# Kernel optimization log

Hardware: AMD Instinct MI355X
Metric: run time of the kernel (lower is better)

The kernel has to match this reference:

```python
import jax, jax.numpy as jnp
import numpy as np

T, A, E, RAW, H, NACT, NTP = 64, 48, 22, 512, 256, 21, 3
# entity_distinct: self entity [0], friendly entities [1:12], hostile entities [12:22]
PARAM_SHAPES = [
    ("W1", (NTP, RAW, H)), ("b1", (NTP, H)), ("W2", (NTP, H, H)), ("b2", (NTP, H)),
    ("WCf", (NTP, 2 * H, H)), ("bCf", (NTP, H)), ("WMf", (NTP, 2 * H + 2 * RAW, H)), ("bMf", (NTP, H)),
    ("WCh", (NTP, 2 * H, H)), ("bCh", (NTP, H)), ("WMh", (NTP, 2 * H + 2 * RAW, H)), ("bMh", (NTP, H)),
    ("L1", (NTP, 2 * H, H)), ("bL1", (NTP, H)), ("L2", (NTP, H, H // 2)), ("bL2", (NTP, H // 2)),
    ("L3", (NTP, H // 2, NACT)), ("bL3", (NTP, NACT)),
    ("V1", (NTP, 2 * H, H)), ("bV1", (NTP, H)), ("V2", (NTP, H, 1)), ("bV2", (NTP, 1)),
]
PNAMES = [n for n, _ in PARAM_SHAPES]


def setup_inputs() -> dict:
    key = jax.random.key(0)
    ks = jax.random.split(key, 3 + len(PARAM_SHAPES))
    inp = {
        "obs": jax.random.normal(ks[0], (T, A, E, RAW), jnp.float32),
        "hete_pick": jax.random.randint(ks[1], (T, A), 0, NTP, jnp.int32),
        "dead": jax.random.bernoulli(ks[2], 0.15, (T, A, E)),
    }
    for i, (n, s) in enumerate(PARAM_SHAPES):
        inp[n] = jax.random.normal(ks[3 + i], s, jnp.float32) * 0.02
    return inp


def _net_forward(p, obs, dead):
    relu = jax.nn.relu
    obs = jnp.where(dead[..., None], 0.0, obs)                    # nan_to_num for dead entities
    v = relu(obs @ p["W1"] + p["b1"]) @ p["W2"] + p["b2"]         # [T,A,E,H] per-entity encoder
    zs, ze_f, ze_h = obs[..., 0, :], obs[..., 1:12, :], obs[..., 12:22, :]
    vs, ve_f, ve_h = v[..., 0, :], v[..., 1:12, :], v[..., 12:22, :]
    df, dh = dead[..., 1:12], dead[..., 12:22]

    def conc(ve, d, ze, WC, bC, WM, bM):
        w = (~d).astype(obs.dtype)                                # alive mask [T,A,Ef]
        denom = jnp.maximum(w.sum(-1, keepdims=True), 1.0)
        pool = jnp.einsum('taeh,tae->tah', ve, w) / denom         # masked mean over entities
        pool_z = jnp.einsum('taer,tae->tar', ze, w) / denom       # skip-connect raw-obs pool
        vC = relu(jnp.concatenate([vs, pool], -1) @ WC + bC)
        vM = relu(jnp.concatenate([vs, pool, zs, pool_z], -1) @ WM + bM)
        return vC, vM

    vfC, vfM = conc(ve_f, df, ze_f, p["WCf"], p["bCf"], p["WMf"], p["bMf"])
    vhC, vhM = conc(ve_h, dh, ze_h, p["WCh"], p["bCh"], p["WMh"], p["bMh"])
    vC = jnp.concatenate([vfC, vhC], -1)                          # [T,A,2H] dual-conc fuse
    vM = jnp.concatenate([vfM, vhM], -1)
    logits = relu(relu(vC @ p["L1"] + p["bL1"]) @ p["L2"] + p["bL2"]) @ p["L3"] + p["bL3"]
    value = relu(vM @ p["V1"] + p["bV1"]) @ p["V2"] + p["bV2"]    # [T,A,1]
    logp = jax.nn.log_softmax(logits, -1)
    act = jnp.argmax(logits, -1)                                  # deterministic (test_mode) action
    alp = jnp.take_along_axis(logp, act[..., None], -1)           # [T,A,1] action log-prob
    return act, value, alp


def reference(obs, hete_pick, dead, W1, b1, W2, b2, WCf, bCf, WMf, bMf, WCh, bCh, WMh, bMh,
              L1, bL1, L2, bL2, L3, bL3, V1, bV1, V2, bV2):
    params = dict(W1=W1, b1=b1, W2=W2, b2=b2, WCf=WCf, bCf=bCf, WMf=WMf, bMf=bMf,
                  WCh=WCh, bCh=bCh, WMh=WMh, bMh=bMh, L1=L1, bL1=bL1, L2=L2, bL2=bL2,
                  L3=L3, bL3=bL3, V1=V1, bV1=bV1, V2=V2, bV2=bV2)
    act = jnp.zeros((T, A), jnp.int32)
    value = jnp.zeros((T, A, 1), obs.dtype)
    alp = jnp.zeros((T, A, 1), obs.dtype)
    for t in range(NTP):                                          # heterogeneous dispatch (distribute_compute)
        pt = {k: v[t] for k, v in params.items()}
        a_t, v_t, lp_t = _net_forward(pt, obs, dead)
        m = hete_pick == t                                        # mask_arr[t]
        act = jnp.where(m, a_t.astype(jnp.int32), act)
        value = jnp.where(m[..., None], v_t, value)
        alp = jnp.where(m[..., None], lp_t, alp)
    return act, value, alp
```

## Files before the change

### kernel.cpp

```cpp
#include <hip/hip_runtime.h>
#include <cstdint>

#define T_ 64
#define A_ 48
#define NP_ 3072
#define E_ 22
#define RAW_ 512
#define H_ 256
#define NACT_ 21
#define NTP_ 3
#define PV_ 3456
#define RV_ 68096
#define NDEAD_ 67584

typedef unsigned short u16;
typedef __attribute__((ext_vector_type(8))) short short8;
typedef __attribute__((ext_vector_type(4))) short short4v;
typedef __attribute__((ext_vector_type(4))) float floatx4;

__device__ __forceinline__ u16 f2bf(float x) {
    unsigned r;
    asm("v_cvt_pk_bf16_f32 %0, %1, %1" : "=v"(r) : "v"(x));
    return (u16)r;
}
__device__ __forceinline__ float bf2f(u16 h) {
    return __uint_as_float(((unsigned)h) << 16);
}

typedef __attribute__((address_space(1))) const void* gp_t;
typedef __attribute__((address_space(3))) void* lp_t;
__device__ __forceinline__ void gload16(const void* g, void* l) {
    __builtin_amdgcn_global_load_lds((gp_t)g, (lp_t)l, 16, 0, 0);
}

__device__ __forceinline__ floatx4 ld_f4(const float* p) {
    floatx4 r;
    asm volatile("global_load_dwordx4 %0, %1, off" : "=&v"(r) : "v"(p));
    return r;
}
__device__ __forceinline__ short8 ld_s8(const u16* p) {
    short8 r;
    asm volatile("global_load_dwordx4 %0, %1, off" : "=&v"(r) : "v"(p));
    return r;
}
template<int N>
__device__ __forceinline__ void wait_vm_f(floatx4 (&a)[4]) {
    asm volatile("s_waitcnt vmcnt(%4)"
                 : "+v"(a[0]), "+v"(a[1]), "+v"(a[2]), "+v"(a[3])
                 : "i"(N) : "memory");
}
template<int N>
__device__ __forceinline__ void wait_vm_s(short8 (&a)[4]) {
    asm volatile("s_waitcnt vmcnt(%4)"
                 : "+v"(a[0]), "+v"(a[1]), "+v"(a[2]), "+v"(a[3])
                 : "i"(N) : "memory");
}

__device__ __forceinline__ int swzk(int r) { return ((r >> 1) ^ r) & 3; }

__global__ void k_bucket(const unsigned* __restrict__ deadRaw,
                         const int* __restrict__ hete, int* __restrict__ wsI)
{
    __shared__ int fl[2];
    __shared__ int sc[3], cur[3], sps[3], srs[3];
    int tid = threadIdx.x;
    if (tid < 2) fl[tid] = 0;
    if (tid < 3) { sc[tid] = 0; cur[tid] = 0; }
    __syncthreads();
    int ni = 0, nf = 0;
    for (int i = tid; i < 1024; i += 256) {
        unsigned w = deadRaw[i];
        if (w > 1u) ni = 1;
        if (w != 0u && w != 0x3F800000u) nf = 1;
    }
    if (ni) atomicOr(&fl[0], 1);
    if (nf) atomicOr(&fl[1], 1);
    for (int p = tid; p < NP_; p += 256) atomicAdd(&sc[hete[p]], 1);
    __syncthreads();
    if (tid == 0) {
        int c0 = sc[0], c1 = sc[1], c2 = sc[2];
        int p1 = (c0 + 127) & ~127;
        int p2 = p1 + ((c1 + 127) & ~127);
        sps[0] = 0; sps[1] = p1; sps[2] = p2;
        int r1 = (22 * c0 + 127) & ~127;
        int r2 = r1 + ((22 * c1 + 127) & ~127);
        srs[0] = 0; srs[1] = r1; srs[2] = r2;
        wsI[0] = fl[0] ? (fl[1] ? 2 : 1) : 0;
        wsI[1] = c0; wsI[2] = c1; wsI[3] = c2;
        wsI[4] = 0; wsI[5] = p1; wsI[6] = p2;
        wsI[8] = 0; wsI[9] = r1; wsI[10] = r2;
    }
    __syncthreads();
    int* pairIdx = wsI + 16;
    int* prb = pairIdx + PV_;
    for (int pv = tid; pv < PV_; pv += 256) pairIdx[pv] = -1;
    __syncthreads();
    for (int p = tid; p < NP_; p += 256) {
        int t = hete[p];
        int pos = atomicAdd(&cur[t], 1);
        pairIdx[sps[t] + pos] = p;
    }
    for (int pv = tid; pv < PV_; pv += 256) {
        int t = (pv >= sps[1]) + (pv >= sps[2]);
        prb[pv] = srs[t] + 22 * (pv - sps[t]);
    }
}

__global__ void k_deadmask(const void* __restrict__ dead,
                           const int* __restrict__ wsI, float* __restrict__ dm)
{
    int i = blockIdx.x * 256 + threadIdx.x;
    if (i >= NDEAD_) return;
    int mode = wsI[0];
    bool d;
    if (mode == 0)      d = ((const int*)dead)[i] != 0;
    else if (mode == 1) d = ((const float*)dead)[i] != 0.f;
    else                d = ((const unsigned char*)dead)[i] != 0;
    dm[i] = d ? 0.f : 1.f;
}

__global__ void k_rowobs(const int* __restrict__ cnt, const int* __restrict__ ps,
                         const int* __restrict__ rs, const int* __restrict__ pairIdx,
                         const float* __restrict__ dm, int* __restrict__ rowObs)
{
    int rv = blockIdx.x * 256 + threadIdx.x;
    if (rv >= RV_) return;
    int t = (rv >= rs[1]) + (rv >= rs[2]);
    int local = rv - rs[t];
    int out = -1;
    if (local < 22 * cnt[t]) {
        int pl = local / 22;
        int e = local - pl * 22;
        int p = pairIdx[ps[t] + pl];
        if (p >= 0) {
            int oi = p * 22 + e;
            if (dm[oi] != 0.f) out = oi;
        }
    }
    rowObs[rv] = out;
}

struct WCA {
    const float* W[8]; u16* Hi[8]; u16* Lo[8]; int K[8]; int bs[9];
};
__global__ __launch_bounds__(256) void k_wconv(WCA a)
{
    int blk = blockIdx.x;
    int s = 0;
#pragma unroll
    for (int i = 1; i < 8; ++i) if (blk >= a.bs[i]) s = i;
    int lb = blk - a.bs[s];
    int K = a.K[s];
    int K8 = K >> 3;
    int kc = lb % K8;
    int t  = lb / K8;
    int n  = threadIdx.x;
    const float* w = a.W[s] + (long)t * K * 256 + n;
    short8 hv, lv;
#pragma unroll
    for (int j = 0; j < 8; ++j) {
        float x = w[(long)(kc * 8 + j) * 256];
        u16 hh = f2bf(x);
        hv[j] = (short)hh;
        lv[j] = (short)f2bf(x - bf2f(hh));
    }
    long o = ((long)t * 256 + n) * K + kc * 8;
    *(short8*)(a.Hi[s] + o) = hv;
    *(short8*)(a.Lo[s] + o) = lv;
}

struct GD {
    const void* Aa; const void* Ab;
    const u16* Bh; const u16* Bl;
    const float* bias;
    void* Ca; void* Cb;
    long lda; long ldc;
    int K; int coff;
};
struct GA4 { GD d[4]; };

template<int AMODE, bool RELU, int OUTS>
__global__ __launch_bounds__(256, 2) void k_mgemm(
    GA4 ga, const int* __restrict__ rowIdx, const int* __restrict__ starts)
{
    __shared__ short smem[32768];
    const int tid = threadIdx.x;
    const GD d = ga.d[blockIdx.z];
    const long rb = (long)blockIdx.x * 128;
    const int n0 = blockIdx.y * 128;
    const int t = (rb >= starts[0]) + (rb >= starts[1]);
    const int K = d.K;
    const long lda = d.lda;
    const u16* bhT = d.Bh + ((long)t * 256 + n0) * K;
    const u16* blT = d.Bl + ((long)t * 256 + n0) * K;
    const float* biasT = d.bias + (long)t * 256 + n0;

    const int cs = tid & 3;
    const int r0 = tid >> 2;
    const int r1 = 64 + r0;

    const int ar = tid >> 3;
    const int ac = (tid & 7) * 4;
    long arow[4]; float amask[4];
    const float* Afp = (const float*)d.Aa;
    if (AMODE == 1) {
#pragma unroll
        for (int it = 0; it < 4; ++it) {
            int r = 32 * it + ar;
            int i0 = rowIdx[rb + r];
            amask[it] = (i0 < 0) ? 0.f : 1.f;
            arow[it] = (i0 < 0) ? 0 : (long)i0 * lda;
        }
    }
    const u16* ahT = (const u16*)d.Aa;
    const u16* alT = (const u16*)d.Ab;

    const int wave = tid >> 6;
    const int lane = tid & 63;
    const int wr = (wave >> 1) * 64;
    const int wc = (wave & 1) * 64;
    const int lm = lane & 15;
    const int quad = lane >> 4;

    auto issueB = [&](int b, int k0) {
        short* Bh = smem + b * 16384 + 8192;
        short* Bl = smem + b * 16384 + 12288;
#pragma unroll
        for (int i = 0; i < 2; ++i) {
            int c = i * 256 + tid;
            int r = c >> 2;
            long go = (long)r * K + k0 + ((cs ^ swzk(r)) << 3);
            gload16(bhT + go, &Bh[c << 3]);
            gload16(blT + go, &Bl[c << 3]);
        }
    };
    auto issueA1 = [&](int k0, floatx4 (&dst)[4]) {
#pragma unroll
        for (int it = 0; it < 4; ++it)
            dst[it] = ld_f4(Afp + arow[it] + k0 + ac);
    };
    auto issueA0 = [&](int k0, short8 (&dst)[4]) {
        dst[0] = ld_s8(ahT + (rb + r0) * lda + k0 + cs * 8);
        dst[1] = ld_s8(ahT + (rb + r1) * lda + k0 + cs * 8);
        dst[2] = ld_s8(alT + (rb + r0) * lda + k0 + cs * 8);
        dst[3] = ld_s8(alT + (rb + r1) * lda + k0 + cs * 8);
    };
    auto writeA1 = [&](int b, floatx4 (&src)[4]) {
        short* AhW = smem + b * 16384;
        short* AlW = AhW + 4096;
#pragma unroll
        for (int it = 0; it < 4; ++it) {
            short4v hv, lv;
#pragma unroll
            for (int e = 0; e < 4; ++e) {
                float x = src[it][e] * amask[it];
                u16 hh = f2bf(x);
                hv[e] = (short)hh;
                lv[e] = (short)f2bf(x - bf2f(hh));
            }
            int r = 32 * it + ar;
            int bs = (((ac >> 3) ^ swzk(r)) << 4) | ((ac & 4) << 1);
            *(short4v*)((char*)AhW + r * 64 + bs) = hv;
            *(short4v*)((char*)AlW + r * 64 + bs) = lv;
        }
    };
    auto writeA0 = [&](int b, short8 (&src)[4]) {
        short* AhW = smem + b * 16384;
        short* AlW = AhW + 4096;
        *(short8*)((char*)AhW + r0 * 64 + ((cs ^ swzk(r0)) << 4)) = src[0];
        *(short8*)((char*)AhW + r1 * 64 + ((cs ^ swzk(r1)) << 4)) = src[1];
        *(short8*)((char*)AlW + r0 * 64 + ((cs ^ swzk(r0)) << 4)) = src[2];
        *(short8*)((char*)AlW + r1 * 64 + ((cs ^ swzk(r1)) << 4)) = src[3];
    };

    floatx4 acc[4][4];
#pragma unroll
    for (int i = 0; i < 4; ++i)
#pragma unroll
        for (int j = 0; j < 4; ++j) acc[i][j] = (floatx4){0.f, 0.f, 0.f, 0.f};

    auto computeT = [&](int b) {
        const short* Ah = smem + b * 16384;
        const short* Al = Ah + 4096;
        const short* Bh = Ah + 8192;
        const short* Bl = Ah + 12288;
        short8 fah[4], fal[4];
#pragma unroll
        for (int i = 0; i < 4; ++i) {
            int m = wr + 16 * i + lm;
            int sl = (quad ^ swzk(m)) << 3;
            fah[i] = *(const short8*)&Ah[(m << 5) + sl];
            fal[i] = *(const short8*)&Al[(m << 5) + sl];
        }
        __builtin_amdgcn_s_setprio(1);
#pragma unroll
        for (int j = 0; j < 4; ++j) {
            int n = wc + 16 * j + lm;
            int sl = (quad ^ swzk(n)) << 3;
            short8 fbh = *(const short8*)&Bh[(n << 5) + sl];
            short8 fbl = *(const short8*)&Bl[(n << 5) + sl];
#pragma unroll
            for (int i = 0; i < 4; ++i) {
                acc[i][j] = __builtin_amdgcn_mfma_f32_16x16x32_bf16(fah[i], fbh, acc[i][j], 0, 0, 0);
                acc[i][j] = __builtin_amdgcn_mfma_f32_16x16x32_bf16(fal[i], fbh, acc[i][j], 0, 0, 0);
                acc[i][j] = __builtin_amdgcn_mfma_f32_16x16x32_bf16(fah[i], fbl, acc[i][j], 0, 0, 0);
            }
        }
        __builtin_amdgcn_s_setprio(0);
    };

    floatx4 fS0[4], fS1[4];
    short8  s0[4], s1[4];
    const int nt = K >> 5;

    if (AMODE == 1) issueA1(0, fS0); else issueA0(0, s0);
    issueB(0, 0);
    if (AMODE == 1) { wait_vm_f<4>(fS0); writeA1(0, fS0); }
    else            { wait_vm_s<4>(s0);  writeA0(0, s0); }
    if (AMODE == 1) issueA1(32, fS1); else issueA0(32, s1);
    asm volatile("s_waitcnt vmcnt(4) lgkmcnt(0)" ::: "memory");
    __builtin_amdgcn_s_barrier();
    __builtin_amdgcn_sched_barrier(0);

    for (int ti = 0; ti < nt; ti += 2) {
        {
            const int kB = ((ti + 1 < nt) ? ti + 1 : nt - 1) << 5;
            const int kA = ((ti + 2 < nt) ? ti + 2 : nt - 1) << 5;
            issueB(1, kB);
            if (AMODE == 1) issueA1(kA, fS0); else issueA0(kA, s0);
            computeT(0);
            if (AMODE == 1) { wait_vm_f<8>(fS1); writeA1(1, fS1); }
            else            { wait_vm_s<8>(s1);  writeA0(1, s1); }
            asm volatile("s_waitcnt vmcnt(4) lgkmcnt(0)" ::: "memory");
            __builtin_amdgcn_s_barrier();
            __builtin_amdgcn_sched_barrier(0);
        }
        {
            const int kB = ((ti + 2 < nt) ? ti + 2 : nt - 1) << 5;
            const int kA = ((ti + 3 < nt) ? ti + 3 : nt - 1) << 5;
            issueB(0, kB);
            if (AMODE == 1) issueA1(kA, fS1); else issueA0(kA, s1);
            computeT(1);
            if (AMODE == 1) { wait_vm_f<8>(fS0); writeA1(0, fS0); }
            else            { wait_vm_s<8>(s0);  writeA0(0, s0); }
            asm volatile("s_waitcnt vmcnt(4) lgkmcnt(0)" ::: "memory");
            __builtin_amdgcn_s_barrier();
            __builtin_amdgcn_sched_barrier(0);
        }
    }
    asm volatile("s_waitcnt vmcnt(0) lgkmcnt(0)" ::: "memory");
    __builtin_amdgcn_s_barrier();
    __builtin_amdgcn_sched_barrier(0);

    if (OUTS == 0) {
        float* C = (float*)d.Ca;
#pragma unroll
        for (int j = 0; j < 4; ++j) {
            int col = wc + 16 * j + lm;
            float bj = biasT[col];
#pragma unroll
            for (int i = 0; i < 4; ++i) {
                long rbase = rb + wr + 16 * i + quad * 4;
#pragma unroll
                for (int r = 0; r < 4; ++r) {
                    float vv = acc[i][j][r] + bj;
                    if (RELU) vv = fmaxf(vv, 0.f);
                    C[(rbase + r) * d.ldc + d.coff + n0 + col] = vv;
                }
            }
        }
    } else {
        u16* Chi = (u16*)smem;
        u16* Clo = Chi + 16384;
#pragma unroll
        for (int j = 0; j < 4; ++j) {
            int col = wc + 16 * j + lm;
            float bj = biasT[col];
#pragma unroll
            for (int i = 0; i < 4; ++i) {
                int row0 = wr + 16 * i + quad * 4;
#pragma unroll
                for (int r = 0; r < 4; ++r) {
                    float vv = acc[i][j][r] + bj;
                    if (RELU) vv = fmaxf(vv, 0.f);
                    int row = row0 + r;
                    int cc = col ^ (((row >> 2) & 3) << 4);
                    u16 hh = f2bf(vv);
                    Chi[row * 128 + cc] = hh;
                    Clo[row * 128 + cc] = f2bf(vv - bf2f(hh));
                }
            }
        }
        asm volatile("s_waitcnt lgkmcnt(0)" ::: "memory");
        __builtin_amdgcn_s_barrier();
        __builtin_amdgcn_sched_barrier(0);
        u16* Ca = (u16*)d.Ca;
        u16* Cb = (u16*)d.Cb;
#pragma unroll
        for (int s = 0; s < 8; ++s) {
            int ch = s * 256 + tid;
            int row = ch >> 4;
            int gcol = (ch & 15) * 8;
            int lo = row * 128 + (gcol ^ (((row >> 2) & 3) << 4));
            short8 hv = *(const short8*)&Chi[lo];
            short8 lv = *(const short8*)&Clo[lo];
            long go = (rb + row) * d.ldc + d.coff + n0 + gcol;
            *(short8*)(Ca + go) = hv;
            *(short8*)(Cb + go) = lv;
        }
    }
}

__global__ __launch_bounds__(256) void k_prep(
    const int* __restrict__ pairIdx, const int* __restrict__ prb,
    const float* __restrict__ dm, const float* __restrict__ v,
    const float* __restrict__ obs,
    u16* __restrict__ XFh, u16* __restrict__ XFl,
    u16* __restrict__ XHh, u16* __restrict__ XHl)
{
    int pv = blockIdx.x, c = threadIdx.x;
    int p = pairIdx[pv];
    long xo = (long)pv * 1536;
    if (p < 0) {
        for (int s = 0; s < 6; ++s) {
            XFh[xo + s * 256 + c] = 0; XFl[xo + s * 256 + c] = 0;
            XHh[xo + s * 256 + c] = 0; XHl[xo + s * 256 + c] = 0;
        }
        return;
    }
    __shared__ float sw[22];
    if (c < 22) sw[c] = dm[p * 22 + c];
    __syncthreads();
    float denf = 0.f, denh = 0.f;
    for (int e = 1; e < 12; ++e)  denf += sw[e];
    for (int e = 12; e < 22; ++e) denh += sw[e];
    denf = 1.f / fmaxf(denf, 1.f);
    denh = 1.f / fmaxf(denh, 1.f);

    auto wsp = [&](u16* Hh, u16* Hl, long idx, float val) {
        u16 hh = f2bf(val);
        Hh[idx] = hh;
        Hl[idx] = f2bf(val - bf2f(hh));
    };

    long base = prb[pv];
    float vs = v[base * 256 + c];
    wsp(XFh, XFl, xo + c, vs);
    wsp(XHh, XHl, xo + c, vs);
    float af = 0.f, ah = 0.f;
    for (int e = 1; e < 12; ++e)  af += sw[e] * v[(base + e) * 256 + c];
    for (int e = 12; e < 22; ++e) ah += sw[e] * v[(base + e) * 256 + c];
    wsp(XFh, XFl, xo + 256 + c, af * denf);
    wsp(XHh, XHl, xo + 256 + c, ah * denh);
    const float* ob = obs + (long)p * 22 * 512;
    float w0 = sw[0];
    float z0 = ob[c] * w0;
    float z1 = ob[256 + c] * w0;
    wsp(XFh, XFl, xo + 512 + c, z0); wsp(XHh, XHl, xo + 512 + c, z0);
    wsp(XFh, XFl, xo + 768 + c, z1); wsp(XHh, XHl, xo + 768 + c, z1);
#pragma unroll
    for (int half = 0; half < 2; ++half) {
        int c2 = c + half * 256;
        float zf = 0.f, zh = 0.f;
        for (int e = 1; e < 12; ++e)  zf += sw[e] * ob[(long)e * 512 + c2];
        for (int e = 12; e < 22; ++e) zh += sw[e] * ob[(long)e * 512 + c2];
        wsp(XFh, XFl, xo + 1024 + c2, zf * denf);
        wsp(XHh, XHl, xo + 1024 + c2, zh * denh);
    }
}

__global__ __launch_bounds__(128) void k_final(
    const float* __restrict__ g1, const float* __restrict__ vV,
    const float* __restrict__ L2, const float* __restrict__ bL2,
    const float* __restrict__ L3, const float* __restrict__ bL3,
    const float* __restrict__ V2, const float* __restrict__ bV2,
    const int* __restrict__ pairIdx, const int* __restrict__ ps,
    float* __restrict__ out)
{
    int pv = blockIdx.x;
    int p = pairIdx[pv];
    if (p < 0) return;
    int c = threadIdx.x;
    int t = (pv >= ps[1]) + (pv >= ps[2]);

    __shared__ float sg1[256], sg2[128], sval[2];
    const float* g1p = g1 + (long)pv * 256;
    sg1[c] = g1p[c];
    sg1[c + 128] = g1p[c + 128];

    const float* vv = vV + (long)pv * 256;
    const float* v2t = V2 + t * 256;
    float s = vv[c] * v2t[c] + vv[c + 128] * v2t[c + 128];
    for (int off = 32; off; off >>= 1) s += __shfl_down(s, off);
    if ((c & 63) == 0) sval[c >> 6] = s;
    __syncthreads();

    const float* l2 = L2 + (long)t * 256 * 128 + c;
    float a = bL2[t * 128 + c];
#pragma unroll 8
    for (int k = 0; k < 256; ++k) a = fmaf(sg1[k], l2[(long)k * 128], a);
    sg2[c] = fmaxf(a, 0.f);
    __syncthreads();

    if (c < 64) {
        float lg = -3.0e38f;
        if (c < 21) {
            const float* l3t = L3 + (long)t * 128 * 21 + c;
            float acc = bL3[t * 21 + c];
            for (int k = 0; k < 128; ++k) acc = fmaf(sg2[k], l3t[k * 21], acc);
            lg = acc;
        }
        float mv = lg; int mi = (c < 21) ? c : 9999;
        for (int off = 32; off; off >>= 1) {
            float ov = __shfl_down(mv, off);
            int oi = __shfl_down(mi, off);
            if (ov > mv || (ov == mv && oi < mi)) { mv = ov; mi = oi; }
        }
        mv = __shfl(mv, 0); mi = __shfl(mi, 0);
        float e = (c < 21) ? expf(lg - mv) : 0.f;
        for (int off = 32; off; off >>= 1) e += __shfl_down(e, off);
        if (c == 0) {
            out[p] = (float)mi;
            out[NP_ + p] = sval[0] + sval[1] + bV2[t];
            out[2 * NP_ + p] = -logf(e);
        }
    }
}

extern "C" void kernel_launch(void* const* d_in, const int* in_sizes, int n_in,
                              void* d_out, int out_size, void* d_ws, size_t ws_size,
                              hipStream_t stream)
{
    const float* obs = (const float*)d_in[0];
    const int* hete = (const int*)d_in[1];
    const void* dead = d_in[2];
    const float* W1 = (const float*)d_in[3];  const float* b1 = (const float*)d_in[4];
    const float* W2 = (const float*)d_in[5];  const float* b2 = (const float*)d_in[6];
    const float* WCf = (const float*)d_in[7]; const float* bCf = (const float*)d_in[8];
    const float* WMf = (const float*)d_in[9]; const float* bMf = (const float*)d_in[10];
    const float* WCh = (const float*)d_in[11]; const float* bCh = (const float*)d_in[12];
    const float* WMh = (const float*)d_in[13]; const float* bMh = (const float*)d_in[14];
    const float* L1 = (const float*)d_in[15]; const float* bL1 = (const float*)d_in[16];
    const float* L2 = (const float*)d_in[17]; const float* bL2 = (const float*)d_in[18];
    const float* L3 = (const float*)d_in[19]; const float* bL3 = (const float*)d_in[20];
    const float* V1 = (const float*)d_in[21]; const float* bV1 = (const float*)d_in[22];
    const float* V2 = (const float*)d_in[23]; const float* bV2 = (const float*)d_in[24];
    float* out = (float*)d_out;

    int* wsI = (int*)d_ws;
    int* pairIdx = wsI + 16;
    int* prb = pairIdx + PV_;
    int* rowObs = prb + PV_;
    long fbase = ((16L + PV_ + PV_ + RV_) + 63) & ~63L;
    float* wsF = (float*)d_ws;
    float* dm = wsF + fbase;
    float* cur = dm + NDEAD_;
    auto allocUS = [&](long K) { u16* p = (u16*)cur; cur += (3L * 256 * K) / 2; return p; };
    u16* W1h = allocUS(512);  u16* W1l = allocUS(512);
    u16* W2h = allocUS(256);  u16* W2l = allocUS(256);
    u16* WCfh = allocUS(512); u16* WCfl = allocUS(512);
    u16* WChh = allocUS(512); u16* WChl = allocUS(512);
    u16* WMfh = allocUS(1536); u16* WMfl = allocUS(1536);
    u16* WMhh = allocUS(1536); u16* WMhl = allocUS(1536);
    u16* L1h = allocUS(512);  u16* L1l = allocUS(512);
    u16* V1h = allocUS(512);  u16* V1l = allocUS(512);
    float* regA = cur;
    float* regB = regA + (long)RV_ * 256;

    u16* h1h = (u16*)regA;
    u16* h1l = h1h + (long)RV_ * 256;
    u16* XFh = (u16*)regA;
    u16* XFl = XFh + (long)PV_ * 1536;
    u16* XHh = XFl + (long)PV_ * 1536;
    u16* XHl = XHh + (long)PV_ * 1536;
    float* v = regB;
    u16* vCh = (u16*)regB;
    u16* vCl = vCh + (long)PV_ * 512;
    u16* vMh = vCl + (long)PV_ * 512;
    u16* vMl = vMh + (long)PV_ * 512;
    float* g1 = (float*)(vMl + (long)PV_ * 512);
    float* vV = g1 + (long)PV_ * 256;

    k_bucket<<<1, 256, 0, stream>>>((const unsigned*)dead, hete, wsI);
    k_deadmask<<<264, 256, 0, stream>>>(dead, wsI, dm);
    k_rowobs<<<266, 256, 0, stream>>>(wsI + 1, wsI + 4, wsI + 8, pairIdx, dm, rowObs);

    {
        WCA wa;
        const float* Ws[8] = {W1, W2, WCf, WCh, WMf, WMh, L1, V1};
        u16* His[8] = {W1h, W2h, WCfh, WChh, WMfh, WMhh, L1h, V1h};
        u16* Los[8] = {W1l, W2l, WCfl, WChl, WMfl, WMhl, L1l, V1l};
        int Ks[8] = {512, 256, 512, 512, 1536, 1536, 512, 512};
        int acc_b = 0; wa.bs[0] = 0;
        for (int i = 0; i < 8; ++i) {
            wa.W[i] = Ws[i]; wa.Hi[i] = His[i]; wa.Lo[i] = Los[i]; wa.K[i] = Ks[i];
            acc_b += 3 * Ks[i] / 8; wa.bs[i + 1] = acc_b;
        }
        k_wconv<<<acc_b, 256, 0, stream>>>(wa);
    }

    GA4 g;
    auto setd = [&](int i, const void* Aa, const void* Ab, const u16* Bh_, const u16* Bl_,
                    const float* bias, void* Ca, void* Cb, long lda_, long ldc_, int K_, int coff_) {
        g.d[i] = GD{Aa, Ab, Bh_, Bl_, bias, Ca, Cb, lda_, ldc_, K_, coff_};
    };

    for (int i = 0; i < 4; ++i)
        setd(i, obs, nullptr, W1h, W1l, b1, h1h, h1l, 512, 256, 512, 0);
    k_mgemm<1, true, 1><<<dim3(RV_ / 128, 2, 1), 256, 0, stream>>>(g, rowObs, wsI + 9);

    for (int i = 0; i < 4; ++i)
        setd(i, h1h, h1l, W2h, W2l, b2, v, nullptr, 256, 256, 256, 0);
    k_mgemm<0, false, 0><<<dim3(RV_ / 128, 2, 1), 256, 0, stream>>>(g, nullptr, wsI + 9);

    k_prep<<<PV_, 256, 0, stream>>>(pairIdx, prb, dm, v, obs, XFh, XFl, XHh, XHl);

    setd(0, XFh, XFl, WCfh, WCfl, bCf, vCh, vCl, 1536, 512, 512, 0);
    setd(1, XHh, XHl, WChh, WChl, bCh, vCh, vCl, 1536, 512, 512, 256);
    setd(2, XFh, XFl, WMfh, WMfl, bMf, vMh, vMl, 1536, 512, 1536, 0);
    setd(3, XHh, XHl, WMhh, WMhl, bMh, vMh, vMl, 1536, 512, 1536, 256);
    k_mgemm<0, true, 1><<<dim3(PV_ / 128, 2, 4), 256, 0, stream>>>(g, nullptr, wsI + 5);

    setd(0, vCh, vCl, L1h, L1l, bL1, g1, nullptr, 512, 256, 512, 0);
    setd(1, vMh, vMl, V1h, V1l, bV1, vV, nullptr, 512, 256, 512, 0);
    setd(2, vCh, vCl, L1h, L1l, bL1, g1, nullptr, 512, 256, 512, 0);
    setd(3, vCh, vCl, L1h, L1l, bL1, g1, nullptr, 512, 256, 512, 0);
    k_mgemm<0, true, 0><<<dim3(PV_ / 128, 2, 2), 256, 0, stream>>>(g, nullptr, wsI + 5);

    k_final<<<PV_, 128, 0, stream>>>(g1, vV, L2, bL2, L3, bL3, V2, bV2,
                                     pairIdx, wsI + 4, out);
    (void)in_sizes; (void)n_in; (void)out_size; (void)ws_size;
}
```

Baseline: 505.7 us.

## Single-buffer GEMM LDS and stage B through registers to raise occupancy

Halves the GEMM kernel's shared memory from two pipeline buffers to one and raises launch bounds from 2 to 3 blocks per CU. B tiles are now loaded into registers with plain global loads and written to LDS after compute, instead of async global_load_lds into a second buffer. The bf16 output staging is split into two 64-row passes so it fits the smaller LDS. The aim is more resident waves to hide latency, at the cost of an extra barrier per k-step, less load/compute overlap within a block, and more register pressure.

```diff
diff --git a/kernel.cpp b/kernel.cpp
--- a/kernel.cpp
+++ b/kernel.cpp
@@ -25,12 +25,6 @@
 }
 __device__ __forceinline__ float bf2f(u16 h) {
     return __uint_as_float(((unsigned)h) << 16);
-}
-
-typedef __attribute__((address_space(1))) const void* gp_t;
-typedef __attribute__((address_space(3))) void* lp_t;
-__device__ __forceinline__ void gload16(const void* g, void* l) {
-    __builtin_amdgcn_global_load_lds((gp_t)g, (lp_t)l, 16, 0, 0);
 }
 
 __device__ __forceinline__ floatx4 ld_f4(const float* p) {
@@ -180,10 +174,10 @@
 struct GA4 { GD d[4]; };
 
 template<int AMODE, bool RELU, int OUTS>
-__global__ __launch_bounds__(256, 2) void k_mgemm(
+__global__ __launch_bounds__(256, 3) void k_mgemm(
     GA4 ga, const int* __restrict__ rowIdx, const int* __restrict__ starts)
 {
-    __shared__ short smem[32768];
+    __shared__ short smem[16384];
     const int tid = threadIdx.x;
     const GD d = ga.d[blockIdx.z];
     const long rb = (long)blockIdx.x * 128;
@@ -222,18 +216,11 @@
     const int lm = lane & 15;
     const int quad = lane >> 4;
 
-    auto issueB = [&](int b, int k0) {
-        short* Bh = smem + b * 16384 + 8192;
-        short* Bl = smem + b * 16384 + 12288;
-#pragma unroll
-        for (int i = 0; i < 2; ++i) {
-            int c = i * 256 + tid;
-            int r = c >> 2;
-            long go = (long)r * K + k0 + ((cs ^ swzk(r)) << 3);
-            gload16(bhT + go, &Bh[c << 3]);
-            gload16(blT + go, &Bl[c << 3]);
-        }
-    };
+    short* AhW = smem;
+    short* AlW = smem + 4096;
+    short* BhW = smem + 8192;
+    short* BlW = smem + 12288;
+
     auto issueA1 = [&](int k0, floatx4 (&dst)[4]) {
 #pragma unroll
         for (int it = 0; it < 4; ++it)
@@ -245,9 +232,13 @@
         dst[2] = ld_s8(alT + (rb + r0) * lda + k0 + cs * 8);
         dst[3] = ld_s8(alT + (rb + r1) * lda + k0 + cs * 8);
     };
-    auto writeA1 = [&](int b, floatx4 (&src)[4]) {
-        short* AhW = smem + b * 16384;
-        short* AlW = AhW + 4096;
+    auto issueB = [&](int k0, short8 (&dst)[4]) {
+        dst[0] = ld_s8(bhT + (long)r0 * K + k0 + cs * 8);
+        dst[1] = ld_s8(bhT + (long)r1 * K + k0 + cs * 8);
+        dst[2] = ld_s8(blT + (long)r0 * K + k0 + cs * 8);
+        dst[3] = ld_s8(blT + (long)r1 * K + k0 + cs * 8);
+    };
+    auto writeA1 = [&](floatx4 (&src)[4]) {
 #pragma unroll
         for (int it = 0; it < 4; ++it) {
             short4v hv, lv;
@@ -264,14 +255,18 @@
             *(short4v*)((char*)AlW + r * 64 + bs) = lv;
         }
     };
-    auto writeA0 = [&](int b, short8 (&src)[4]) {
-        short* AhW = smem + b * 16384;
-        short* AlW = AhW + 4096;
+    auto writeA0 = [&](short8 (&src)[4]) {
         *(short8*)((char*)AhW + r0 * 64 + ((cs ^ swzk(r0)) << 4)) = src[0];
         *(short8*)((char*)AhW + r1 * 64 + ((cs ^ swzk(r1)) << 4)) = src[1];
         *(short8*)((char*)AlW + r0 * 64 + ((cs ^ swzk(r0)) << 4)) = src[2];
         *(short8*)((char*)AlW + r1 * 64 + ((cs ^ swzk(r1)) << 4)) = src[3];
     };
+    auto writeB = [&](short8 (&src)[4]) {
+        *(short8*)((char*)BhW + r0 * 64 + ((cs ^ swzk(r0)) << 4)) = src[0];
+        *(short8*)((char*)BhW + r1 * 64 + ((cs ^ swzk(r1)) << 4)) = src[1];
+        *(short8*)((char*)BlW + r0 * 64 + ((cs ^ swzk(r0)) << 4)) = src[2];
+        *(short8*)((char*)BlW + r1 * 64 + ((cs ^ swzk(r1)) << 4)) = src[3];
+    };
 
     floatx4 acc[4][4];
 #pragma unroll
@@ -279,26 +274,22 @@
 #pragma unroll
         for (int j = 0; j < 4; ++j) acc[i][j] = (floatx4){0.f, 0.f, 0.f, 0.f};
 
-    auto computeT = [&](int b) {
-        const short* Ah = smem + b * 16384;
-        const short* Al = Ah + 4096;
-        const short* Bh = Ah + 8192;
-        const short* Bl = Ah + 12288;
+    auto computeT = [&]() {
         short8 fah[4], fal[4];
 #pragma unroll
         for (int i = 0; i < 4; ++i) {
             int m = wr + 16 * i + lm;
             int sl = (quad ^ swzk(m)) << 3;
-            fah[i] = *(const short8*)&Ah[(m << 5) + sl];
-            fal[i] = *(const short8*)&Al[(m << 5) + sl];
+            fah[i] = *(const short8*)&AhW[(m << 5) + sl];
+            fal[i] = *(const short8*)&AlW[(m << 5) + sl];
         }
         __builtin_amdgcn_s_setprio(1);
 #pragma unroll
         for (int j = 0; j < 4; ++j) {
             int n = wc + 16 * j + lm;
             int sl = (quad ^ swzk(n)) << 3;
-            short8 fbh = *(const short8*)&Bh[(n << 5) + sl];
-            short8 fbl = *(const short8*)&Bl[(n << 5) + sl];
+            short8 fbh = *(const short8*)&BhW[(n << 5) + sl];
+            short8 fbl = *(const short8*)&BlW[(n << 5) + sl];
 #pragma unroll
             for (int i = 0; i < 4; ++i) {
                 acc[i][j] = __builtin_amdgcn_mfma_f32_16x16x32_bf16(fah[i], fbh, acc[i][j], 0, 0, 0);
@@ -309,48 +300,33 @@
         __builtin_amdgcn_s_setprio(0);
     };
 
-    floatx4 fS0[4], fS1[4];
-    short8  s0[4], s1[4];
+    floatx4 fS[4];
+    short8  sA[4], sB[4];
     const int nt = K >> 5;
 
-    if (AMODE == 1) issueA1(0, fS0); else issueA0(0, s0);
-    issueB(0, 0);
-    if (AMODE == 1) { wait_vm_f<4>(fS0); writeA1(0, fS0); }
-    else            { wait_vm_s<4>(s0);  writeA0(0, s0); }
-    if (AMODE == 1) issueA1(32, fS1); else issueA0(32, s1);
-    asm volatile("s_waitcnt vmcnt(4) lgkmcnt(0)" ::: "memory");
+    if (AMODE == 1) issueA1(0, fS); else issueA0(0, sA);
+    issueB(0, sB);
+    if (AMODE == 1) { wait_vm_f<4>(fS); writeA1(fS); }
+    else            { wait_vm_s<4>(sA); writeA0(sA); }
+    wait_vm_s<0>(sB); writeB(sB);
+    asm volatile("s_waitcnt lgkmcnt(0)" ::: "memory");
     __builtin_amdgcn_s_barrier();
     __builtin_amdgcn_sched_barrier(0);
 
-    for (int ti = 0; ti < nt; ti += 2) {
-        {
-            const int kB = ((ti + 1 < nt) ? ti + 1 : nt - 1) << 5;
-            const int kA = ((ti + 2 < nt) ? ti + 2 : nt - 1) << 5;
-            issueB(1, kB);
-            if (AMODE == 1) issueA1(kA, fS0); else issueA0(kA, s0);
-            computeT(0);
-            if (AMODE == 1) { wait_vm_f<8>(fS1); writeA1(1, fS1); }
-            else            { wait_vm_s<8>(s1);  writeA0(1, s1); }
-            asm volatile("s_waitcnt vmcnt(4) lgkmcnt(0)" ::: "memory");
-            __builtin_amdgcn_s_barrier();
-            __builtin_amdgcn_sched_barrier(0);
-        }
-        {
-            const int kB = ((ti + 2 < nt) ? ti + 2 : nt - 1) << 5;
-            const int kA = ((ti + 3 < nt) ? ti + 3 : nt - 1) << 5;
-            issueB(0, kB);
-            if (AMODE == 1) issueA1(kA, fS1); else issueA0(kA, s1);
-            computeT(1);
-            if (AMODE == 1) { wait_vm_f<8>(fS0); writeA1(0, fS0); }
-            else            { wait_vm_s<8>(s0);  writeA0(0, s0); }
-            asm volatile("s_waitcnt vmcnt(4) lgkmcnt(0)" ::: "memory");
-            __builtin_amdgcn_s_barrier();
-            __builtin_amdgcn_sched_barrier(0);
-        }
-    }
-    asm volatile("s_waitcnt vmcnt(0) lgkmcnt(0)" ::: "memory");
-    __builtin_amdgcn_s_barrier();
-    __builtin_amdgcn_sched_barrier(0);
+    for (int ti = 0; ti < nt; ++ti) {
+        const int kn = ((ti + 1 < nt) ? ti + 1 : nt - 1) << 5;
+        if (AMODE == 1) issueA1(kn, fS); else issueA0(kn, sA);
+        issueB(kn, sB);
+        computeT();
+        __builtin_amdgcn_s_barrier();
+        __builtin_amdgcn_sched_barrier(0);
+        if (AMODE == 1) { wait_vm_f<4>(fS); writeA1(fS); }
+        else            { wait_vm_s<4>(sA); writeA0(sA); }
+        wait_vm_s<0>(sB); writeB(sB);
+        asm volatile("s_waitcnt lgkmcnt(0)" ::: "memory");
+        __builtin_amdgcn_s_barrier();
+        __builtin_amdgcn_sched_barrier(0);
+    }
 
     if (OUTS == 0) {
         float* C = (float*)d.Ca;
@@ -371,42 +347,52 @@
         }
     } else {
         u16* Chi = (u16*)smem;
-        u16* Clo = Chi + 16384;
-#pragma unroll
-        for (int j = 0; j < 4; ++j) {
-            int col = wc + 16 * j + lm;
-            float bj = biasT[col];
-#pragma unroll
-            for (int i = 0; i < 4; ++i) {
-                int row0 = wr + 16 * i + quad * 4;
-#pragma unroll
-                for (int r = 0; r < 4; ++r) {
-                    float vv = acc[i][j][r] + bj;
-                    if (RELU) vv = fmaxf(vv, 0.f);
-                    int row = row0 + r;
-                    int cc = col ^ (((row >> 2) & 3) << 4);
-                    u16 hh = f2bf(vv);
-                    Chi[row * 128 + cc] = hh;
-                    Clo[row * 128 + cc] = f2bf(vv - bf2f(hh));
+        u16* Clo = Chi + 8192;
+        u16* Ca = (u16*)d.Ca;
+        u16* Cb = (u16*)d.Cb;
+#pragma unroll
+        for (int pass = 0; pass < 2; ++pass) {
+            if ((wr >> 6) == pass) {
+#pragma unroll
+                for (int j = 0; j < 4; ++j) {
+                    int col = wc + 16 * j + lm;
+                    float bj = biasT[col];
+#pragma unroll
+                    for (int i = 0; i < 4; ++i) {
+                        int lrow0 = 16 * i + quad * 4;
+#pragma unroll
+                        for (int r = 0; r < 4; ++r) {
+                            float vv = acc[i][j][r] + bj;
+                            if (RELU) vv = fmaxf(vv, 0.f);
+                            int row = lrow0 + r;
+                            int cc = col ^ (((row >> 2) & 3) << 4);
+                            u16 hh = f2bf(vv);
+                            Chi[row * 128 + cc] = hh;
+                            Clo[row * 128 + cc] = f2bf(vv - bf2f(hh));
+                        }
+                    }
                 }
             }
-        }
-        asm volatile("s_waitcnt lgkmcnt(0)" ::: "memory");
-        __builtin_amdgcn_s_barrier();
-        __builtin_amdgcn_sched_barrier(0);
-        u16* Ca = (u16*)d.Ca;
-        u16* Cb = (u16*)d.Cb;
-#pragma unroll
-        for (int s = 0; s < 8; ++s) {
-            int ch = s * 256 + tid;
-            int row = ch >> 4;
-            int gcol = (ch & 15) * 8;
-            int lo = row * 128 + (gcol ^ (((row >> 2) & 3) << 4));
-            short8 hv = *(const short8*)&Chi[lo];
-            short8 lv = *(const short8*)&Clo[lo];
-            long go = (rb + row) * d.ldc + d.coff + n0 + gcol;
-            *(short8*)(Ca + go) = hv;
-            *(short8*)(Cb + go) = lv;
+            asm volatile("s_waitcnt lgkmcnt(0)" ::: "memory");
+            __builtin_amdgcn_s_barrier();
+            __builtin_amdgcn_sched_barrier(0);
+#pragma unroll
+            for (int s = 0; s < 4; ++s) {
+                int ch = s * 256 + tid;
+                int row = ch >> 4;
+                int gcol = (ch & 15) * 8;
+                int lo = row * 128 + (gcol ^ (((row >> 2) & 3) << 4));
+                short8 hv = *(const short8*)&Chi[lo];
+                short8 lv = *(const short8*)&Clo[lo];
+                long go = (rb + pass * 64 + row) * d.ldc + d.coff + n0 + gcol;
+                *(short8*)(Ca + go) = hv;
+                *(short8*)(Cb + go) = lv;
+            }
+            if (pass == 0) {
+                asm volatile("s_waitcnt lgkmcnt(0)" ::: "memory");
+                __builtin_amdgcn_s_barrier();
+                __builtin_amdgcn_sched_barrier(0);
+            }
         }
     }
 }
```

Measured after the change: 523.6 us. +3.5%, slower.
